# Performance work log

Measured on AMD Instinct MI355X. Metric: run time of the kernel, lower is better.

Reference implementation:

```python
import jax, jax.numpy as jnp
import numpy as np

N_NODES = 100000
N_EDGES = 1600000
F_IN = 512


def setup_inputs() -> dict:
    key = jax.random.key(0)
    ks = jax.random.split(key, 12)
    x = jax.random.normal(ks[0], (N_NODES, F_IN), dtype=jnp.float32)
    edge_index = jax.random.randint(ks[1], (2, N_EDGES), 0, N_NODES, dtype=jnp.int64)
    def glorot(k, fan_in, fan_out):
        lim = np.sqrt(6.0 / (fan_in + fan_out)).astype(np.float32)
        return jax.random.uniform(k, (fan_in, fan_out), jnp.float32, -lim, lim)
    return {
        "x": x,
        "edge_index": edge_index,
        "W1": glorot(ks[2], F_IN, 64), "b1": jnp.zeros((64,), jnp.float32),
        "W2": glorot(ks[3], 64, 32),   "b2": jnp.zeros((32,), jnp.float32),
        "W3": glorot(ks[4], 32, 16),   "b3": jnp.zeros((16,), jnp.float32),
        "Wl": glorot(ks[5], 16, 7),    "bl": jnp.zeros((7,), jnp.float32),
    }


def _gcn_conv(x, W, b, src, dst, norm, n_nodes):
    # GCNConv: h = W^T x, then symmetric-normalized scatter-add aggregation
    h = x @ W                                  # [N, out]
    msg = h[src] * norm[:, None]               # gather + edge-normalize [E', out]
    agg = jax.ops.segment_sum(msg, dst, num_segments=n_nodes)  # scatter-add
    return agg + b


def reference(x, edge_index, W1, b1, W2, b2, W3, b3, Wl, bl):
    n = x.shape[0]
    loop = jnp.arange(n, dtype=edge_index.dtype)
    # add self-loops (PyG GCNConv default)
    src = jnp.concatenate([edge_index[0], loop])
    dst = jnp.concatenate([edge_index[1], loop])
    deg = jax.ops.segment_sum(jnp.ones_like(dst, dtype=x.dtype), dst, num_segments=n)
    dis = jnp.where(deg > 0, jax.lax.rsqrt(deg), 0.0)  # deg^{-1/2}
    norm = dis[src] * dis[dst]                          # [E']

    # dropout is identity in eval mode
    h = jax.nn.relu(_gcn_conv(x, W1, b1, src, dst, norm, n))
    h = jax.nn.relu(_gcn_conv(h, W2, b2, src, dst, norm, n))
    h = _gcn_conv(h, W3, b3, src, dst, norm, n)
    return h @ Wl + bl                                   # [N, 7]
```

## Files before the change

### kernel.cpp

```cpp
#include <hip/hip_runtime.h>


typedef __bf16 bf16x8 __attribute__((ext_vector_type(8)));
typedef short short8v __attribute__((ext_vector_type(8)));
typedef unsigned short ushort8v __attribute__((ext_vector_type(8)));
typedef unsigned short ushort4v __attribute__((ext_vector_type(4)));
typedef float float4v __attribute__((ext_vector_type(4)));

static inline int ceil_div_i(long long a, long long b) { return (int)((a + b - 1) / b); }

#define CAP 16384
#define SCHUNK 8192
#define RPB 128

#define GLOAD_LDS16(gsrc, ldst)                                                  \
    __builtin_amdgcn_global_load_lds(                                            \
        (const __attribute__((address_space(1))) unsigned*)(gsrc),               \
        (__attribute__((address_space(3))) unsigned*)(ldst), 16, 0, 0)

__device__ inline unsigned short bf16rne(float f) {
    union { float f; unsigned u; } c; c.f = f;
    unsigned u = c.u;
    u += 0x7fffu + ((u >> 16) & 1u);
    return (unsigned short)(u >> 16);
}
__device__ inline float bf16tof(unsigned short h) {
    return __uint_as_float((unsigned)h << 16);
}

__global__ __launch_bounds__(256) void init_kernel(const float* __restrict__ W1,
                                                   unsigned short* __restrict__ wt,
                                                   int* __restrict__ gtail) {
    const int t = threadIdx.x;
    if (blockIdx.x == 0) gtail[t] = t * CAP;
    for (int i = blockIdx.x * 256 + t; i < 512 * 64; i += gridDim.x * 256) {
        int k = i >> 6, n = i & 63;
        wt[(size_t)n * 512 + k] = bf16rne(W1[i]);
    }
}

__global__ __launch_bounds__(256) void scatter_gemm1_kernel(
        const int* __restrict__ src, const int* __restrict__ dst,
        int* __restrict__ gtail, unsigned* __restrict__ abuf, int E, int EB,
        const float* __restrict__ x, const unsigned short* __restrict__ wt,
        unsigned short* __restrict__ g1, int M) {
    __shared__ int cur[256];
    __shared__ __align__(16) char xs[RPB * 32 * 4];
    __shared__ __align__(16) unsigned short wst[64 * 40];
    const int t = threadIdx.x;
    if (blockIdx.x < EB) {
        const int e0 = blockIdx.x * SCHUNK;
        const int e1 = min(e0 + SCHUNK, E);
        cur[t] = 0;
        __syncthreads();
        for (int e = e0 + t; e < e1; e += 256) atomicAdd(&cur[dst[e] >> 9], 1);
        __syncthreads();
        int c = cur[t];
        cur[t] = c ? atomicAdd(&gtail[t], c) : 0;
        __syncthreads();
        for (int e = e0 + t; e < e1; e += 256) {
            int d = dst[e];
            int pos = atomicAdd(&cur[d >> 9], 1);
            abuf[pos] = ((unsigned)(d & 511) << 23) | (unsigned)src[e];
        }
        return;
    }
    const int tile = blockIdx.x - EB;
    const int w = t >> 6, l = t & 63;
    const int lr = l & 15, g = l >> 4;
    const int row0 = tile * RPB;
    float4v acc[2][4] = {};

    for (int c = 0; c < 16; ++c) {
        const int k0 = c * 32;
        if (c) __syncthreads();
        {
            char* ldsb = xs + w * 4096;
            #pragma unroll
            for (int j = 0; j < 4; ++j) {
                int o = w * 4096 + j * 1024 + l * 16;
                int r = o >> 7;
                int colb = (o & 127) ^ ((r & 7) << 4);
                int grow = row0 + r;
                if (grow >= M) grow = 0;
                const char* gs = (const char*)x + (size_t)grow * 2048 +
                                 (size_t)k0 * 4 + colb;
                GLOAD_LDS16(gs, ldsb + j * 1024);
            }
        }
        {
            int n = t >> 2, q = t & 3;
            ushort8v v = *(const ushort8v*)(wt + (size_t)n * 512 + k0 + q * 8);
            *(ushort8v*)&wst[n * 40 + q * 8] = v;
        }
        __syncthreads();
        bf16x8 bf[4];
        #pragma unroll
        for (int f = 0; f < 4; ++f)
            bf[f] = *(const bf16x8*)&wst[(f * 16 + lr) * 40 + g * 8];
        #pragma unroll
        for (int st = 0; st < 2; ++st) {
            const int r = w * 32 + st * 16 + lr;
            const int swz = (r & 7) << 4;
            const char* base = xs + r * 128;
            float4 xa = *(const float4*)(base + ((g * 32) ^ swz));
            float4 xb = *(const float4*)(base + ((g * 32 + 16) ^ swz));
            short8v av;
            av[0] = (short)bf16rne(xa.x); av[1] = (short)bf16rne(xa.y);
            av[2] = (short)bf16rne(xa.z); av[3] = (short)bf16rne(xa.w);
            av[4] = (short)bf16rne(xb.x); av[5] = (short)bf16rne(xb.y);
            av[6] = (short)bf16rne(xb.z); av[7] = (short)bf16rne(xb.w);
            bf16x8 a = __builtin_bit_cast(bf16x8, av);
            #pragma unroll
            for (int f = 0; f < 4; ++f)
                acc[st][f] = __builtin_amdgcn_mfma_f32_16x16x32_bf16(a, bf[f],
                                                                     acc[st][f], 0, 0, 0);
        }
    }
    #pragma unroll
    for (int st = 0; st < 2; ++st) {
        const int ro0 = row0 + w * 32 + st * 16 + 4 * g;
        #pragma unroll
        for (int r = 0; r < 4; ++r) {
            int ro = ro0 + r;
            if (ro < M) {
                #pragma unroll
                for (int f = 0; f < 4; ++f)
                    g1[(size_t)ro * 64 + f * 16 + lr] = bf16rne(acc[st][f][r]);
            }
        }
    }
}

__global__ __launch_bounds__(256) void build_kernel(const int* __restrict__ gtail,
                                                    const unsigned* __restrict__ abuf,
                                                    int* __restrict__ row_start,
                                                    int* __restrict__ row_end,
                                                    float* __restrict__ dis,
                                                    int* __restrict__ csr_src, int M) {
    __shared__ int hist[512];
    __shared__ int cur[512];
    __shared__ int wsum_[4];
    const int b = blockIdx.x, t = threadIdx.x, lane = t & 63, wid = t >> 6;
    const int n0 = b << 9;
    const int s = b * CAP;
    const int e = gtail[b];
    hist[t] = 0; hist[t + 256] = 0;
    __syncthreads();
    for (int i = s + t; i < e; i += 256) atomicAdd(&hist[abuf[i] >> 23], 1);
    __syncthreads();
    int c0 = hist[2 * t], c1 = hist[2 * t + 1];
    int pair = c0 + c1;
    int inc = pair;
    #pragma unroll
    for (int d = 1; d < 64; d <<= 1) {
        int o = __shfl_up(inc, d);
        if (lane >= d) inc += o;
    }
    if (lane == 63) wsum_[wid] = inc;
    __syncthreads();
    int wpre = 0;
    for (int ww = 0; ww < wid; ++ww) wpre += wsum_[ww];
    int excl = wpre + inc - pair;
    int r0 = s + excl, r1 = r0 + c0;
    int n = n0 + 2 * t;
    if (n < M) {
        row_start[n] = r0; row_end[n] = r1;
        dis[n] = rsqrtf((float)(c0 + 1));
    }
    if (n + 1 < M) {
        row_start[n + 1] = r1; row_end[n + 1] = r1 + c1;
        dis[n + 1] = rsqrtf((float)(c1 + 1));
    }
    cur[2 * t] = r0; cur[2 * t + 1] = r1;
    __syncthreads();
    for (int i = s + t; i < e; i += 256) {
        unsigned p = abuf[i];
        int pos = atomicAdd(&cur[p >> 23], 1);
        csr_src[pos] = (int)(p & 0x7fffffu);
    }
}

template <int F, int FOUT, int LPN, bool RELU, bool FINAL, bool EDGEW>
__global__ __launch_bounds__(256) void gather_mlp_kernel(
        const int* __restrict__ row_start, const int* __restrict__ row_end,
        const int* __restrict__ csr_src, const float* __restrict__ dis,
        const unsigned short* __restrict__ gin, const float* __restrict__ bin,
        const float* __restrict__ W, const float* __restrict__ bout,
        void* __restrict__ o_, int M) {
    constexpr int VEC = F / LPN;
    constexpr int NPB = 256 / LPN;
    constexpr int HSS = F + 4;
    __shared__ float Ws[F * FOUT];
    __shared__ float hs[NPB][HSS];
    __shared__ float bs[FINAL ? FOUT : 1];
    const int t = threadIdx.x;
    for (int i = t; i < F * FOUT; i += 256) Ws[i] = W[i];
    if (FINAL && t < FOUT) bs[t] = bout[t];
    const int grp = t / LPN, gl = t % LPN;
    const int n = blockIdx.x * NPB + grp;
    float dn = 0.f;
    if (n < M) {
        const int rs = row_start[n], re = row_end[n];
        dn = dis[n];
        float acc[VEC] = {};
        int i = rs;
        while (i < re) {
            const int take = re - i;
            int s = 0; float wl = 0.f;
            if (gl < take) {
                s = csr_src[i + gl];
                if constexpr (EDGEW) wl = dis[s];
            }
            #pragma unroll
            for (int jj = 0; jj < LPN; ++jj) {
                if (jj < take) {
                    int sj = __shfl(s, jj, LPN);
                    float wj;
                    if constexpr (EDGEW) wj = __shfl(wl, jj, LPN) * dn;
                    if constexpr (VEC == 8) {
                        ushort8v r8 = *(const ushort8v*)(gin + (size_t)sj * F + gl * 8);
                        #pragma unroll
                        for (int k = 0; k < 8; ++k) {
                            float v = bf16tof(r8[k]);
                            if constexpr (EDGEW) acc[k] += wj * v; else acc[k] += v;
                        }
                    } else {
                        ushort4v r4 = *(const ushort4v*)(gin + (size_t)sj * F + gl * 4);
                        #pragma unroll
                        for (int k = 0; k < 4; ++k) {
                            float v = bf16tof(r4[k]);
                            if constexpr (EDGEW) acc[k] += wj * v; else acc[k] += v;
                        }
                    }
                }
            }
            i += LPN;
        }
        const float sw = EDGEW ? dn * dn : 1.f;
        if constexpr (VEC == 8) {
            ushort8v r8 = *(const ushort8v*)(gin + (size_t)n * F + gl * 8);
            #pragma unroll
            for (int k = 0; k < 8; ++k) acc[k] += sw * bf16tof(r8[k]);
        } else {
            ushort4v r4 = *(const ushort4v*)(gin + (size_t)n * F + gl * 4);
            #pragma unroll
            for (int k = 0; k < 4; ++k) acc[k] += sw * bf16tof(r4[k]);
        }
        #pragma unroll
        for (int k = 0; k < VEC; ++k) {
            float pre = EDGEW ? acc[k] : dn * acc[k];
            float r = pre + bin[gl * VEC + k];
            if (RELU) r = fmaxf(r, 0.f);
            hs[grp][gl * VEC + k] = r;
        }
    }
    __syncthreads();
    if (!FINAL) {
        constexpr int OCPT = FOUT / LPN;
        if (n < M) {
            const int oc0 = gl * OCPT;
            float a[OCPT] = {};
            #pragma unroll
            for (int k = 0; k < F; ++k) {
                float hv = hs[grp][k];
                if constexpr (OCPT == 4) {
                    float4 wv = *(const float4*)&Ws[k * FOUT + oc0];
                    a[0] += hv * wv.x; a[1] += hv * wv.y;
                    a[2] += hv * wv.z; a[3] += hv * wv.w;
                } else {
                    float2 wv = *(const float2*)&Ws[k * FOUT + oc0];
                    a[0] += hv * wv.x; a[1] += hv * wv.y;
                }
            }
            unsigned short* o = (unsigned short*)o_;
            if constexpr (OCPT == 4) {
                ushort4v pk;
                #pragma unroll
                for (int j = 0; j < 4; ++j) pk[j] = bf16rne(a[j] * dn);
                *(ushort4v*)(o + (size_t)n * FOUT + oc0) = pk;
            } else {
                #pragma unroll
                for (int j = 0; j < OCPT; ++j)
                    o[(size_t)n * FOUT + oc0 + j] = bf16rne(a[j] * dn);
            }
        }
    } else {
        float* o = (float*)o_;
        for (int idx = t; idx < NPB * FOUT; idx += 256) {
            int nl = idx / FOUT, oc = idx % FOUT;
            int nn = blockIdx.x * NPB + nl;
            if (nn >= M) continue;
            float a = bs[oc];
            #pragma unroll
            for (int k = 0; k < F; ++k) a += hs[nl][k] * Ws[k * FOUT + oc];
            o[(size_t)nn * FOUT + oc] = a;
        }
    }
}

extern "C" void kernel_launch(void* const* d_in, const int* in_sizes, int n_in,
                              void* d_out, int out_size, void* d_ws, size_t ws_size,
                              hipStream_t stream) {
    const float* x  = (const float*)d_in[0];
    const int* eidx = (const int*)d_in[1];
    const float* W1 = (const float*)d_in[2];
    const float* b1 = (const float*)d_in[3];
    const float* W2 = (const float*)d_in[4];
    const float* b2 = (const float*)d_in[5];
    const float* W3 = (const float*)d_in[6];
    const float* b3 = (const float*)d_in[7];
    const float* Wl = (const float*)d_in[8];
    const float* bl = (const float*)d_in[9];
    float* out = (float*)d_out;

    const int M = in_sizes[0] / 512;
    const int E = in_sizes[1] / 2;
    const int* src = eidx;
    const int* dst = eidx + E;
    const int NB = ceil_div_i(M, 512);
    const int EB = ceil_div_i(E, SCHUNK);
    const int NT = ceil_div_i(M, RPB);

    char* ws = (char*)d_ws;
    const size_t szM1 = ((size_t)(M + 1) * 4 + 255) & ~(size_t)255;
    const size_t szAR = ((size_t)NB * CAP * 4 + 255) & ~(size_t)255;
    size_t off = 0;
    int*      gtail     = (int*)(ws + off); off += 1024;
    int*      row_start = (int*)(ws + off); off += szM1;
    int*      row_end   = (int*)(ws + off); off += szM1;
    float*    dis       = (float*)(ws + off); off += szM1;
    unsigned* abuf      = (unsigned*)(ws + off); off += szAR;
    int*      csr_src   = (int*)(ws + off); off += szAR;
    unsigned short* wt  = (unsigned short*)(ws + off); off += 66560;
    unsigned short* g1  = (unsigned short*)(ws + off);
    off += ((size_t)M * 64 * 2 + 255) & ~(size_t)255;
    unsigned short* g2  = (unsigned short*)(ws + off);
    off += ((size_t)M * 32 * 2 + 255) & ~(size_t)255;
    unsigned short* g3  = (unsigned short*)(ws + off);
    off += ((size_t)M * 16 * 2 + 255) & ~(size_t)255;

    init_kernel<<<128, 256, 0, stream>>>(W1, wt, gtail);
    scatter_gemm1_kernel<<<EB + NT, 256, 0, stream>>>(src, dst, gtail, abuf, E, EB,
                                                      x, wt, g1, M);
    build_kernel<<<NB, 256, 0, stream>>>(gtail, abuf, row_start, row_end, dis, csr_src, M);

    gather_mlp_kernel<64, 32, 8, true, false, true><<<ceil_div_i(M, 32), 256, 0, stream>>>(
        row_start, row_end, csr_src, dis, g1, b1, W2, nullptr, g2, M);
    gather_mlp_kernel<32, 16, 8, true, false, false><<<ceil_div_i(M, 32), 256, 0, stream>>>(
        row_start, row_end, csr_src, dis, g2, b2, W3, nullptr, g3, M);
    gather_mlp_kernel<16, 7, 4, false, true, false><<<ceil_div_i(M, 64), 256, 0, stream>>>(
        row_start, row_end, csr_src, dis, g3, b3, Wl, bl, out, M);
}
```

Baseline: 180.4 us.

## Split fused scatter/GEMM1 kernel and vectorize edge scatter with smaller chunks

Splits the combined edge-bucketing and first-layer GEMM kernel into two separate launches, so the scatter blocks no longer carry the GEMM's LDS footprint. The edge chunk per block shrinks from 8192 to 2048, giving more, smaller scatter blocks, and full chunks load src/dst as int4 vectors with unrolled LDS atomics. The cost is losing the overlap between scatter and GEMM work inside one launch, adding an extra kernel launch, and making more global atomics on the bucket tails.

Measured after the change: 194.8 us. 7.9% more time.

```diff
diff --git a/kernel.cpp b/kernel.cpp
--- a/kernel.cpp
+++ b/kernel.cpp
@@ -10,7 +10,7 @@
 static inline int ceil_div_i(long long a, long long b) { return (int)((a + b - 1) / b); }
 
 #define CAP 16384
-#define SCHUNK 8192
+#define SCHUNK 2048
 #define RPB 128
 
 #define GLOAD_LDS16(gsrc, ldst)                                                  \
@@ -39,20 +39,39 @@
     }
 }
 
-__global__ __launch_bounds__(256) void scatter_gemm1_kernel(
-        const int* __restrict__ src, const int* __restrict__ dst,
-        int* __restrict__ gtail, unsigned* __restrict__ abuf, int E, int EB,
-        const float* __restrict__ x, const unsigned short* __restrict__ wt,
-        unsigned short* __restrict__ g1, int M) {
+__global__ __launch_bounds__(256) void scatter_kernel(const int* __restrict__ src,
+                                                      const int* __restrict__ dst,
+                                                      int* __restrict__ gtail,
+                                                      unsigned* __restrict__ abuf, int E) {
     __shared__ int cur[256];
-    __shared__ __align__(16) char xs[RPB * 32 * 4];
-    __shared__ __align__(16) unsigned short wst[64 * 40];
     const int t = threadIdx.x;
-    if (blockIdx.x < EB) {
-        const int e0 = blockIdx.x * SCHUNK;
-        const int e1 = min(e0 + SCHUNK, E);
-        cur[t] = 0;
-        __syncthreads();
+    const int e0 = blockIdx.x * SCHUNK;
+    const int e1 = min(e0 + SCHUNK, E);
+    cur[t] = 0;
+    __syncthreads();
+    if (e1 - e0 == SCHUNK) {
+        const int4* d4 = (const int4*)(dst + e0);
+        const int4* s4 = (const int4*)(src + e0);
+        int4 d0 = d4[t], d1 = d4[t + 256];
+        atomicAdd(&cur[d0.x >> 9], 1); atomicAdd(&cur[d0.y >> 9], 1);
+        atomicAdd(&cur[d0.z >> 9], 1); atomicAdd(&cur[d0.w >> 9], 1);
+        atomicAdd(&cur[d1.x >> 9], 1); atomicAdd(&cur[d1.y >> 9], 1);
+        atomicAdd(&cur[d1.z >> 9], 1); atomicAdd(&cur[d1.w >> 9], 1);
+        __syncthreads();
+        int c = cur[t];
+        cur[t] = c ? atomicAdd(&gtail[t], c) : 0;
+        __syncthreads();
+        int4 s0 = s4[t], s1 = s4[t + 256];
+        int pos;
+        pos = atomicAdd(&cur[d0.x >> 9], 1); abuf[pos] = ((unsigned)(d0.x & 511) << 23) | (unsigned)s0.x;
+        pos = atomicAdd(&cur[d0.y >> 9], 1); abuf[pos] = ((unsigned)(d0.y & 511) << 23) | (unsigned)s0.y;
+        pos = atomicAdd(&cur[d0.z >> 9], 1); abuf[pos] = ((unsigned)(d0.z & 511) << 23) | (unsigned)s0.z;
+        pos = atomicAdd(&cur[d0.w >> 9], 1); abuf[pos] = ((unsigned)(d0.w & 511) << 23) | (unsigned)s0.w;
+        pos = atomicAdd(&cur[d1.x >> 9], 1); abuf[pos] = ((unsigned)(d1.x & 511) << 23) | (unsigned)s1.x;
+        pos = atomicAdd(&cur[d1.y >> 9], 1); abuf[pos] = ((unsigned)(d1.y & 511) << 23) | (unsigned)s1.y;
+        pos = atomicAdd(&cur[d1.z >> 9], 1); abuf[pos] = ((unsigned)(d1.z & 511) << 23) | (unsigned)s1.z;
+        pos = atomicAdd(&cur[d1.w >> 9], 1); abuf[pos] = ((unsigned)(d1.w & 511) << 23) | (unsigned)s1.w;
+    } else {
         for (int e = e0 + t; e < e1; e += 256) atomicAdd(&cur[dst[e] >> 9], 1);
         __syncthreads();
         int c = cur[t];
@@ -63,12 +82,18 @@
             int pos = atomicAdd(&cur[d >> 9], 1);
             abuf[pos] = ((unsigned)(d & 511) << 23) | (unsigned)src[e];
         }
-        return;
-    }
-    const int tile = blockIdx.x - EB;
+    }
+}
+
+__global__ __launch_bounds__(256) void gemm1_kernel(const float* __restrict__ x,
+                                                    const unsigned short* __restrict__ wt,
+                                                    unsigned short* __restrict__ g1, int M) {
+    __shared__ __align__(16) char xs[RPB * 32 * 4];
+    __shared__ __align__(16) unsigned short wst[64 * 40];
+    const int t = threadIdx.x;
     const int w = t >> 6, l = t & 63;
     const int lr = l & 15, g = l >> 4;
-    const int row0 = tile * RPB;
+    const int row0 = blockIdx.x * RPB;
     float4v acc[2][4] = {};
 
     for (int c = 0; c < 16; ++c) {
@@ -341,8 +366,8 @@
     off += ((size_t)M * 16 * 2 + 255) & ~(size_t)255;
 
     init_kernel<<<128, 256, 0, stream>>>(W1, wt, gtail);
-    scatter_gemm1_kernel<<<EB + NT, 256, 0, stream>>>(src, dst, gtail, abuf, E, EB,
-                                                      x, wt, g1, M);
+    scatter_kernel<<<EB, 256, 0, stream>>>(src, dst, gtail, abuf, E);
+    gemm1_kernel<<<NT, 256, 0, stream>>>(x, wt, g1, M);
     build_kernel<<<NB, 256, 0, stream>>>(gtail, abuf, row_start, row_end, dis, csr_src, M);
 
     gather_mlp_kernel<64, 32, 8, true, false, true><<<ceil_div_i(M, 32), 256, 0, stream>>>(
```

## Pre-convert x to bf16 in scatter kernel and fuse CSR build into GEMM1

Applied to the files above, without the earlier changes.

Adds a grid-stride pass that converts x from fp32 to a bf16 copy, run in the same launch as the edge bucketing. GEMM1 then streams the half-width bf16 rows through LDS and reads W1 fragments straight from global memory instead of staging them in LDS. The CSR build blocks are merged into the GEMM1 launch, which removes one kernel launch and lets build overlap with the GEMM. The cost is extra memory traffic: x is read once in fp32 and the bf16 copy is written and read again, plus a large new workspace buffer.

Result: slower. 261.8 us (+45.1%).

```diff
diff --git a/kernel.cpp b/kernel.cpp
--- a/kernel.cpp
+++ b/kernel.cpp
@@ -12,6 +12,7 @@
 #define CAP 16384
 #define SCHUNK 8192
 #define RPB 128
+#define CVB 2048
 
 #define GLOAD_LDS16(gsrc, ldst)                                                  \
     __builtin_amdgcn_global_load_lds(                                            \
@@ -39,17 +40,14 @@
     }
 }
 
-__global__ __launch_bounds__(256) void scatter_gemm1_kernel(
+__global__ __launch_bounds__(256) void convert_scatter_kernel(
+        const float* __restrict__ x, unsigned short* __restrict__ xb, long long n4,
         const int* __restrict__ src, const int* __restrict__ dst,
-        int* __restrict__ gtail, unsigned* __restrict__ abuf, int E, int EB,
-        const float* __restrict__ x, const unsigned short* __restrict__ wt,
-        unsigned short* __restrict__ g1, int M) {
+        int* __restrict__ gtail, unsigned* __restrict__ abuf, int E) {
     __shared__ int cur[256];
-    __shared__ __align__(16) char xs[RPB * 32 * 4];
-    __shared__ __align__(16) unsigned short wst[64 * 40];
     const int t = threadIdx.x;
-    if (blockIdx.x < EB) {
-        const int e0 = blockIdx.x * SCHUNK;
+    if (blockIdx.x >= CVB) {
+        const int e0 = (blockIdx.x - CVB) * SCHUNK;
         const int e1 = min(e0 + SCHUNK, E);
         cur[t] = 0;
         __syncthreads();
@@ -65,14 +63,78 @@
         }
         return;
     }
-    const int tile = blockIdx.x - EB;
+    const float4* x4 = (const float4*)x;
+    ushort4v* o4 = (ushort4v*)xb;
+    long long i = (long long)blockIdx.x * 256 + t;
+    const long long stride = (long long)CVB * 256;
+    for (; i < n4; i += stride) {
+        float4 v = x4[i];
+        ushort4v pk;
+        pk[0] = bf16rne(v.x); pk[1] = bf16rne(v.y);
+        pk[2] = bf16rne(v.z); pk[3] = bf16rne(v.w);
+        o4[i] = pk;
+    }
+}
+
+__global__ __launch_bounds__(256) void gemm1_build_kernel(
+        const unsigned short* __restrict__ xb, const unsigned short* __restrict__ wt,
+        unsigned short* __restrict__ g1, int M, int NT,
+        const int* __restrict__ gtail, const unsigned* __restrict__ abuf,
+        int* __restrict__ row_start, int* __restrict__ row_end,
+        float* __restrict__ dis, int* __restrict__ csr_src) {
+    __shared__ __align__(16) char xs[RPB * 128];
+    __shared__ int hist[512];
+    __shared__ int curb[512];
+    __shared__ int wsum_[4];
+    const int t = threadIdx.x;
+    if (blockIdx.x >= NT) {
+        const int b = blockIdx.x - NT;
+        const int lane = t & 63, wid = t >> 6;
+        const int n0 = b << 9;
+        const int s = b * CAP;
+        const int e = gtail[b];
+        hist[t] = 0; hist[t + 256] = 0;
+        __syncthreads();
+        for (int i = s + t; i < e; i += 256) atomicAdd(&hist[abuf[i] >> 23], 1);
+        __syncthreads();
+        int c0 = hist[2 * t], c1 = hist[2 * t + 1];
+        int pair = c0 + c1;
+        int inc = pair;
+        #pragma unroll
+        for (int d = 1; d < 64; d <<= 1) {
+            int o = __shfl_up(inc, d);
+            if (lane >= d) inc += o;
+        }
+        if (lane == 63) wsum_[wid] = inc;
+        __syncthreads();
+        int wpre = 0;
+        for (int ww = 0; ww < wid; ++ww) wpre += wsum_[ww];
+        int excl = wpre + inc - pair;
+        int r0 = s + excl, r1 = r0 + c0;
+        int n = n0 + 2 * t;
+        if (n < M) {
+            row_start[n] = r0; row_end[n] = r1;
+            dis[n] = rsqrtf((float)(c0 + 1));
+        }
+        if (n + 1 < M) {
+            row_start[n + 1] = r1; row_end[n + 1] = r1 + c1;
+            dis[n + 1] = rsqrtf((float)(c1 + 1));
+        }
+        curb[2 * t] = r0; curb[2 * t + 1] = r1;
+        __syncthreads();
+        for (int i = s + t; i < e; i += 256) {
+            unsigned p = abuf[i];
+            int pos = atomicAdd(&curb[p >> 23], 1);
+            csr_src[pos] = (int)(p & 0x7fffffu);
+        }
+        return;
+    }
     const int w = t >> 6, l = t & 63;
     const int lr = l & 15, g = l >> 4;
-    const int row0 = tile * RPB;
+    const int row0 = blockIdx.x * RPB;
+    const unsigned short* wp = wt + (size_t)lr * 512 + g * 8;
     float4v acc[2][4] = {};
-
-    for (int c = 0; c < 16; ++c) {
-        const int k0 = c * 32;
+    for (int c = 0; c < 8; ++c) {
         if (c) __syncthreads();
         {
             char* ldsb = xs + w * 4096;
@@ -80,41 +142,28 @@
             for (int j = 0; j < 4; ++j) {
                 int o = w * 4096 + j * 1024 + l * 16;
                 int r = o >> 7;
-                int colb = (o & 127) ^ ((r & 7) << 4);
+                int cb = (o & 127) ^ ((r & 7) << 4);
                 int grow = row0 + r;
                 if (grow >= M) grow = 0;
-                const char* gs = (const char*)x + (size_t)grow * 2048 +
-                                 (size_t)k0 * 4 + colb;
+                const char* gs = (const char*)xb + (size_t)grow * 1024 + c * 128 + cb;
                 GLOAD_LDS16(gs, ldsb + j * 1024);
             }
         }
-        {
-            int n = t >> 2, q = t & 3;
-            ushort8v v = *(const ushort8v*)(wt + (size_t)n * 512 + k0 + q * 8);
-            *(ushort8v*)&wst[n * 40 + q * 8] = v;
-        }
-        __syncthreads();
-        bf16x8 bf[4];
+        __syncthreads();
         #pragma unroll
-        for (int f = 0; f < 4; ++f)
-            bf[f] = *(const bf16x8*)&wst[(f * 16 + lr) * 40 + g * 8];
-        #pragma unroll
-        for (int st = 0; st < 2; ++st) {
-            const int r = w * 32 + st * 16 + lr;
-            const int swz = (r & 7) << 4;
-            const char* base = xs + r * 128;
-            float4 xa = *(const float4*)(base + ((g * 32) ^ swz));
-            float4 xb = *(const float4*)(base + ((g * 32 + 16) ^ swz));
-            short8v av;
-            av[0] = (short)bf16rne(xa.x); av[1] = (short)bf16rne(xa.y);
-            av[2] = (short)bf16rne(xa.z); av[3] = (short)bf16rne(xa.w);
-            av[4] = (short)bf16rne(xb.x); av[5] = (short)bf16rne(xb.y);
-            av[6] = (short)bf16rne(xb.z); av[7] = (short)bf16rne(xb.w);
-            bf16x8 a = __builtin_bit_cast(bf16x8, av);
-            #pragma unroll
-            for (int f = 0; f < 4; ++f)
-                acc[st][f] = __builtin_amdgcn_mfma_f32_16x16x32_bf16(a, bf[f],
-                                                                     acc[st][f], 0, 0, 0);
+        for (int ks = 0; ks < 2; ++ks) {
+            #pragma unroll
+            for (int st = 0; st < 2; ++st) {
+                const int lrow = w * 32 + st * 16 + lr;
+                const int swz = (lrow & 7) << 4;
+                bf16x8 a = *(const bf16x8*)(xs + lrow * 128 + ((ks * 64 + g * 16) ^ swz));
+                #pragma unroll
+                for (int f = 0; f < 4; ++f) {
+                    bf16x8 b = *(const bf16x8*)(wp + f * 8192 + c * 64 + ks * 32);
+                    acc[st][f] = __builtin_amdgcn_mfma_f32_16x16x32_bf16(a, b,
+                                                                         acc[st][f], 0, 0, 0);
+                }
+            }
         }
     }
     #pragma unroll
@@ -129,55 +178,6 @@
                     g1[(size_t)ro * 64 + f * 16 + lr] = bf16rne(acc[st][f][r]);
             }
         }
-    }
-}
-
-__global__ __launch_bounds__(256) void build_kernel(const int* __restrict__ gtail,
-                                                    const unsigned* __restrict__ abuf,
-                                                    int* __restrict__ row_start,
-                                                    int* __restrict__ row_end,
-                                                    float* __restrict__ dis,
-                                                    int* __restrict__ csr_src, int M) {
-    __shared__ int hist[512];
-    __shared__ int cur[512];
-    __shared__ int wsum_[4];
-    const int b = blockIdx.x, t = threadIdx.x, lane = t & 63, wid = t >> 6;
-    const int n0 = b << 9;
-    const int s = b * CAP;
-    const int e = gtail[b];
-    hist[t] = 0; hist[t + 256] = 0;
-    __syncthreads();
-    for (int i = s + t; i < e; i += 256) atomicAdd(&hist[abuf[i] >> 23], 1);
-    __syncthreads();
-    int c0 = hist[2 * t], c1 = hist[2 * t + 1];
-    int pair = c0 + c1;
-    int inc = pair;
-    #pragma unroll
-    for (int d = 1; d < 64; d <<= 1) {
-        int o = __shfl_up(inc, d);
-        if (lane >= d) inc += o;
-    }
-    if (lane == 63) wsum_[wid] = inc;
-    __syncthreads();
-    int wpre = 0;
-    for (int ww = 0; ww < wid; ++ww) wpre += wsum_[ww];
-    int excl = wpre + inc - pair;
-    int r0 = s + excl, r1 = r0 + c0;
-    int n = n0 + 2 * t;
-    if (n < M) {
-        row_start[n] = r0; row_end[n] = r1;
-        dis[n] = rsqrtf((float)(c0 + 1));
-    }
-    if (n + 1 < M) {
-        row_start[n + 1] = r1; row_end[n + 1] = r1 + c1;
-        dis[n + 1] = rsqrtf((float)(c1 + 1));
-    }
-    cur[2 * t] = r0; cur[2 * t + 1] = r1;
-    __syncthreads();
-    for (int i = s + t; i < e; i += 256) {
-        unsigned p = abuf[i];
-        int pos = atomicAdd(&cur[p >> 23], 1);
-        csr_src[pos] = (int)(p & 0x7fffffu);
     }
 }
 
@@ -339,12 +339,17 @@
     off += ((size_t)M * 32 * 2 + 255) & ~(size_t)255;
     unsigned short* g3  = (unsigned short*)(ws + off);
     off += ((size_t)M * 16 * 2 + 255) & ~(size_t)255;
+    unsigned short* xb  = (unsigned short*)(ws + off);
+    off += ((size_t)M * 512 * 2 + 255) & ~(size_t)255;
+
+    const long long n4 = (long long)M * 512 / 4;
 
     init_kernel<<<128, 256, 0, stream>>>(W1, wt, gtail);
-    scatter_gemm1_kernel<<<EB + NT, 256, 0, stream>>>(src, dst, gtail, abuf, E, EB,
-                                                      x, wt, g1, M);
-    build_kernel<<<NB, 256, 0, stream>>>(gtail, abuf, row_start, row_end, dis, csr_src, M);
-
+    convert_scatter_kernel<<<CVB + EB, 256, 0, stream>>>(x, xb, n4, src, dst,
+                                                         gtail, abuf, E);
+    gemm1_build_kernel<<<NT + NB, 256, 0, stream>>>(xb, wt, g1, M, NT,
+                                                    gtail, abuf, row_start,
+                                                    row_end, dis, csr_src);
     gather_mlp_kernel<64, 32, 8, true, false, true><<<ceil_div_i(M, 32), 256, 0, stream>>>(
         row_start, row_end, csr_src, dis, g1, b1, W2, nullptr, g2, M);
     gather_mlp_kernel<32, 16, 8, true, false, false><<<ceil_div_i(M, 32), 256, 0, stream>>>(
```
